# Kernel tuning notes

Hardware: AMD Instinct MI355X
Metric: run time of the kernel (lower is better)

Reference implementation:

```python
import jax, jax.numpy as jnp
import numpy as np

N_NODES = 50000
N_EDGES = 1600000
IN_DIM = 256
HID = 128
HEADS = 1
N_CLASSES = 40
NEG_SLOPE = 0.2


def gat_conv(x, W, a_src, a_dst, b, src, dst, concat):
    """PyG GATConv (eval mode). x: [N, F_in]; W: [H*C, F_in]; a_*: [H, C]; b: bias."""
    N = x.shape[0]
    H, C = a_src.shape
    h = (x @ W.T).reshape(N, H, C)                       # [N, H, C]
    alpha_src = jnp.sum(h * a_src, axis=-1)              # [N, H]
    alpha_dst = jnp.sum(h * a_dst, axis=-1)              # [N, H]
    e = jax.nn.leaky_relu(alpha_src[src] + alpha_dst[dst], NEG_SLOPE)  # [E, H]
    # scatter-softmax over incoming edges of each destination node
    m = jax.ops.segment_max(e, dst, num_segments=N)
    m = jnp.where(jnp.isfinite(m), m, 0.0)               # nodes with no in-edges
    ex = jnp.exp(e - m[dst])
    denom = jax.ops.segment_sum(ex, dst, num_segments=N)
    alpha = ex / jnp.maximum(denom[dst], 1e-16)          # [E, H]
    out = jax.ops.segment_sum(h[src] * alpha[..., None], dst, num_segments=N)  # [N, H, C]
    out = out.reshape(N, H * C) if concat else out.mean(axis=1)
    return out + b


def setup_inputs() -> dict:
    key = jax.random.key(0)
    ks = jax.random.split(key, 10)
    glorot = lambda k, shape: jax.random.normal(k, shape, jnp.float32) * np.sqrt(2.0 / (shape[0] + shape[-1]))
    x = jax.random.normal(ks[0], (N_NODES, IN_DIM), jnp.float32)
    edge_index = jax.random.randint(ks[1], (2, N_EDGES), 0, N_NODES, jnp.int64)
    # layer 0: in=IN_DIM -> hidden, heads=HEADS, concat=True
    W0 = glorot(ks[2], (HEADS * HID, IN_DIM))
    a_src0 = glorot(ks[3], (HEADS, HID))
    a_dst0 = glorot(ks[4], (HEADS, HID))
    b0 = jnp.zeros((HEADS * HID,), jnp.float32)
    # layer 1: in=hidden*heads -> n_classes, concat=False
    W1 = glorot(ks[5], (HEADS * N_CLASSES, HEADS * HID))
    a_src1 = glorot(ks[6], (HEADS, N_CLASSES))
    a_dst1 = glorot(ks[7], (HEADS, N_CLASSES))
    b1 = jnp.zeros((N_CLASSES,), jnp.float32)
    return {"x": x, "edge_index": edge_index,
            "W0": W0, "a_src0": a_src0, "a_dst0": a_dst0, "b0": b0,
            "W1": W1, "a_src1": a_src1, "a_dst1": a_dst1, "b1": b1}


def reference(x, edge_index, W0, a_src0, a_dst0, b0, W1, a_src1, a_dst1, b1):
    N = x.shape[0]
    # PyG GATConv default add_self_loops=True (each layer adds them transiently)
    loop = jnp.arange(N, dtype=edge_index.dtype)
    src = jnp.concatenate([edge_index[0], loop])
    dst = jnp.concatenate([edge_index[1], loop])
    h = gat_conv(x, W0, a_src0, a_dst0, b0, src, dst, concat=True)
    h = jax.nn.relu(h)  # dropout is identity in eval mode
    out = gat_conv(h, W1, a_src1, a_dst1, b1, src, dst, concat=False)
    return out
```

## Files before the change

kernel.cpp:

```cpp
#include <hip/hip_runtime.h>
#include <hip/hip_bf16.h>

#define N_NODES 50000
#define N_EDGES 1600000
#define ET (N_EDGES + N_NODES)
#define IN_DIM 256
#define HID 128
#define NCLS 40
#define NEG 0.2f
#define NBUCK 391
#define CHUNK 8192
#define CAP 5120

typedef short bf16x8 __attribute__((ext_vector_type(8)));
typedef float f32x4  __attribute__((ext_vector_type(4)));

__device__ __forceinline__ unsigned pk2(float a, float b) {
    __hip_bfloat16 ha = __float2bfloat16(a), hb = __float2bfloat16(b);
    unsigned short ua = *(unsigned short*)&ha, ub = *(unsigned short*)&hb;
    return (unsigned)ua | ((unsigned)ub << 16);
}
__device__ __forceinline__ float blo(unsigned u) { return __uint_as_float(u << 16); }
__device__ __forceinline__ float bhi(unsigned u) { return __uint_as_float(u & 0xffff0000u); }

__global__ void k_init(int* __restrict__ cursor) {
    int i = blockIdx.x * 256 + threadIdx.x;
    if (i < NBUCK) cursor[i] = i * CAP;
}

__global__ __launch_bounds__(256) void k_bin_scatter(const int* __restrict__ ei,
                                                     int* __restrict__ cursor,
                                                     unsigned int* __restrict__ buf) {
    __shared__ int sd[CHUNK];
    __shared__ int hist[NBUCK];
    __shared__ int wbase[NBUCK];
    int t = threadIdx.x;
    for (int i = t; i < NBUCK; i += 256) hist[i] = 0;
    __syncthreads();
    int base = blockIdx.x * CHUNK;
    #pragma unroll
    for (int j = 0; j < 32; ++j) {
        int i = base + j * 256 + t;
        int d = -1;
        if (i < ET) d = (i < N_EDGES) ? ei[N_EDGES + i] : (i - N_EDGES);
        sd[j * 256 + t] = d;
        if (d >= 0) atomicAdd(&hist[d >> 7], 1);
    }
    __syncthreads();
    for (int i = t; i < NBUCK; i += 256) {
        int h = hist[i];
        wbase[i] = h ? atomicAdd(&cursor[i], h) : 0;
        hist[i] = 0;
    }
    __syncthreads();
    #pragma unroll
    for (int j = 0; j < 32; ++j) {
        int i = base + j * 256 + t;
        int d = sd[j * 256 + t];
        if (d >= 0) {
            int s_ = (i < N_EDGES) ? ei[i] : d;
            int b = d >> 7;
            int off = atomicAdd(&hist[b], 1);
            buf[wbase[b] + off] = ((unsigned)(d & 127) << 16) | (unsigned)s_;
        }
    }
}

__global__ __launch_bounds__(512) void k_bin_scan(const int* __restrict__ cursor,
                                                  int* __restrict__ cstart,
                                                  int* __restrict__ rp) {
    __shared__ int s[512];
    int t = threadIdx.x;
    int v = (t < NBUCK) ? (cursor[t] - t * CAP) : 0;
    s[t] = v;
    __syncthreads();
    for (int off = 1; off < 512; off <<= 1) {
        int u = (t >= off) ? s[t - off] : 0;
        __syncthreads();
        s[t] += u;
        __syncthreads();
    }
    int ex = s[t] - v;
    if (t < NBUCK) cstart[t] = ex;
    if (t == 0) rp[N_NODES] = ET;
}

__global__ __launch_bounds__(256) void k_bucket_build(const unsigned int* __restrict__ buf,
                                                      const int* __restrict__ cursor,
                                                      const int* __restrict__ cstart,
                                                      int* __restrict__ rp,
                                                      int* __restrict__ csr) {
    __shared__ int cnt[128], rpl[128], cur[128];
    int b = blockIdx.x;
    int t = threadIdx.x;
    int lo = b * CAP, hi = cursor[b];
    int g = cstart[b];
    if (t < 128) cnt[t] = 0;
    __syncthreads();
    for (int i = lo + t; i < hi; i += 256) atomicAdd(&cnt[buf[i] >> 16], 1);
    __syncthreads();
    if (t == 0) {
        int run = 0;
        #pragma unroll
        for (int l = 0; l < 128; ++l) { rpl[l] = run; run += cnt[l]; }
    }
    __syncthreads();
    if (t < 128) {
        int node = b * 128 + t;
        if (node < N_NODES) rp[node] = g + rpl[t];
        cur[t] = 0;
    }
    __syncthreads();
    for (int i = lo + t; i < hi; i += 256) {
        unsigned v = buf[i];
        int dl = v >> 16;
        int off = atomicAdd(&cur[dl], 1);
        csr[g + rpl[dl] + off] = (int)(v & 0xffffu);
    }
}

__global__ __launch_bounds__(256) void k_gemm0(
    const float* __restrict__ x, const float* __restrict__ W0,
    const float* __restrict__ a_s, const float* __restrict__ a_d,
    unsigned short* __restrict__ h0b, float* __restrict__ as0, float* __restrict__ ad0) {
    __shared__ unsigned sA[64 * 36];
    __shared__ unsigned sB[128 * 36];
    int t = threadIdx.x;
    int n0 = blockIdx.x * 64;
    int w = t >> 6, lane = t & 63;
    int rw = lane & 15, q = lane >> 4;
    f32x4 acc[8];
    #pragma unroll
    for (int n = 0; n < 8; ++n) acc[n] = (f32x4){0.f, 0.f, 0.f, 0.f};

    for (int kc = 0; kc < IN_DIM; kc += 64) {
        #pragma unroll
        for (int i = 0; i < 4; ++i) {
            int f = i * 256 + t;
            int r = f >> 4, fq = f & 15;
            float4 v = make_float4(0.f, 0.f, 0.f, 0.f);
            if (n0 + r < N_NODES)
                v = *(const float4*)&x[(size_t)(n0 + r) * IN_DIM + kc + fq * 4];
            *(uint2*)&sA[r * 36 + fq * 2] = make_uint2(pk2(v.x, v.y), pk2(v.z, v.w));
        }
        #pragma unroll
        for (int i = 0; i < 8; ++i) {
            int f = i * 256 + t;
            int c = f >> 4, fq = f & 15;
            float4 v = *(const float4*)&W0[(size_t)c * IN_DIM + kc + fq * 4];
            *(uint2*)&sB[c * 36 + fq * 2] = make_uint2(pk2(v.x, v.y), pk2(v.z, v.w));
        }
        __syncthreads();
        #pragma unroll
        for (int ks = 0; ks < 2; ++ks) {
            bf16x8 af = *(const bf16x8*)((const unsigned short*)sA + (16 * w + rw) * 72 + ks * 32 + q * 8);
            #pragma unroll
            for (int n = 0; n < 8; ++n) {
                bf16x8 bfr = *(const bf16x8*)((const unsigned short*)sB + (n * 16 + rw) * 72 + ks * 32 + q * 8);
                acc[n] = __builtin_amdgcn_mfma_f32_16x16x32_bf16(af, bfr, acc[n], 0, 0, 0);
            }
        }
        __syncthreads();
    }

    float asv[8], adv[8];
    #pragma unroll
    for (int n = 0; n < 8; ++n) { asv[n] = a_s[n * 16 + rw]; adv[n] = a_d[n * 16 + rw]; }
    float ps[4] = {0.f, 0.f, 0.f, 0.f}, pd[4] = {0.f, 0.f, 0.f, 0.f};
    #pragma unroll
    for (int n = 0; n < 8; ++n)
        #pragma unroll
        for (int reg = 0; reg < 4; ++reg) {
            float vv = acc[n][reg];
            ps[reg] += vv * asv[n];
            pd[reg] += vv * adv[n];
        }
    #pragma unroll
    for (int reg = 0; reg < 4; ++reg) {
        int node = n0 + 16 * w + q * 4 + reg;
        if (node < N_NODES) {
            #pragma unroll
            for (int n = 0; n < 8; ++n) {
                __hip_bfloat16 hb = __float2bfloat16(acc[n][reg]);
                h0b[(size_t)node * HID + n * 16 + rw] = *(unsigned short*)&hb;
            }
        }
    }
    #pragma unroll
    for (int reg = 0; reg < 4; ++reg)
        #pragma unroll
        for (int off = 1; off < 16; off <<= 1) {
            ps[reg] += __shfl_xor(ps[reg], off);
            pd[reg] += __shfl_xor(pd[reg], off);
        }
    if (rw == 0) {
        #pragma unroll
        for (int reg = 0; reg < 4; ++reg) {
            int node = n0 + 16 * w + q * 4 + reg;
            if (node < N_NODES) { as0[node] = ps[reg]; ad0[node] = pd[reg]; }
        }
    }
}

__global__ __launch_bounds__(256) void k_agg0(
    const uint4* __restrict__ h0q, const float* __restrict__ as, const float* __restrict__ ad,
    const int* __restrict__ rp, const int* __restrict__ csr,
    const float* __restrict__ bias, unsigned short* __restrict__ actb) {
    __shared__ float sw_[4][64];
    __shared__ int   ss_[4][64];
    int wid = threadIdx.x >> 6, lane = threadIdx.x & 63;
    int q = lane >> 4, ql = lane & 15;
    int node = blockIdx.x * 4 + wid;
    int start = rp[node], end = rp[node + 1];
    float ad_n = ad[node];
    float a0 = 0.f, a1 = 0.f, a2 = 0.f, a3 = 0.f;
    float a4 = 0.f, a5 = 0.f, a6 = 0.f, a7 = 0.f, den = 0.f;
    for (int base = start; base < end; base += 64) {
        int mm = end - base; if (mm > 64) mm = 64;
        int s_l = 0; float w_l = 0.f;
        if (lane < mm) {
            s_l = csr[base + lane];
            float e = as[s_l] + ad_n;
            e = (e > 0.f) ? e : NEG * e;
            w_l = __expf(e);
            den += w_l;
        }
        ss_[wid][lane] = s_l;
        sw_[wid][lane] = w_l;
        for (int jj = 0; jj < mm; jj += 16) {
            int i0 = jj + q, i1 = i0 + 4, i2 = i0 + 8, i3 = i0 + 12;
            int   s0 = ss_[wid][i0], s1 = ss_[wid][i1], s2 = ss_[wid][i2], s3 = ss_[wid][i3];
            float w0 = sw_[wid][i0], w1 = sw_[wid][i1], w2 = sw_[wid][i2], w3 = sw_[wid][i3];
            uint4 u0 = h0q[(size_t)s0 * 16 + ql];
            uint4 u1 = h0q[(size_t)s1 * 16 + ql];
            uint4 u2 = h0q[(size_t)s2 * 16 + ql];
            uint4 u3 = h0q[(size_t)s3 * 16 + ql];
            a0 += w0 * blo(u0.x) + w1 * blo(u1.x) + w2 * blo(u2.x) + w3 * blo(u3.x);
            a1 += w0 * bhi(u0.x) + w1 * bhi(u1.x) + w2 * bhi(u2.x) + w3 * bhi(u3.x);
            a2 += w0 * blo(u0.y) + w1 * blo(u1.y) + w2 * blo(u2.y) + w3 * blo(u3.y);
            a3 += w0 * bhi(u0.y) + w1 * bhi(u1.y) + w2 * bhi(u2.y) + w3 * bhi(u3.y);
            a4 += w0 * blo(u0.z) + w1 * blo(u1.z) + w2 * blo(u2.z) + w3 * blo(u3.z);
            a5 += w0 * bhi(u0.z) + w1 * bhi(u1.z) + w2 * bhi(u2.z) + w3 * bhi(u3.z);
            a6 += w0 * blo(u0.w) + w1 * blo(u1.w) + w2 * blo(u2.w) + w3 * blo(u3.w);
            a7 += w0 * bhi(u0.w) + w1 * bhi(u1.w) + w2 * bhi(u2.w) + w3 * bhi(u3.w);
        }
    }
    #pragma unroll
    for (int off = 32; off; off >>= 1) den += __shfl_xor(den, off);
    a0 += __shfl_xor(a0, 16); a0 += __shfl_xor(a0, 32);
    a1 += __shfl_xor(a1, 16); a1 += __shfl_xor(a1, 32);
    a2 += __shfl_xor(a2, 16); a2 += __shfl_xor(a2, 32);
    a3 += __shfl_xor(a3, 16); a3 += __shfl_xor(a3, 32);
    a4 += __shfl_xor(a4, 16); a4 += __shfl_xor(a4, 32);
    a5 += __shfl_xor(a5, 16); a5 += __shfl_xor(a5, 32);
    a6 += __shfl_xor(a6, 16); a6 += __shfl_xor(a6, 32);
    a7 += __shfl_xor(a7, 16); a7 += __shfl_xor(a7, 32);
    if (lane < 16) {
        float inv = 1.f / fmaxf(den, 1e-16f);
        float4 b0v = *(const float4*)&bias[ql * 8];
        float4 b1v = *(const float4*)&bias[ql * 8 + 4];
        float r0 = fmaxf(a0 * inv + b0v.x, 0.f);
        float r1 = fmaxf(a1 * inv + b0v.y, 0.f);
        float r2 = fmaxf(a2 * inv + b0v.z, 0.f);
        float r3 = fmaxf(a3 * inv + b0v.w, 0.f);
        float r4 = fmaxf(a4 * inv + b1v.x, 0.f);
        float r5 = fmaxf(a5 * inv + b1v.y, 0.f);
        float r6 = fmaxf(a6 * inv + b1v.z, 0.f);
        float r7 = fmaxf(a7 * inv + b1v.w, 0.f);
        *(uint4*)&actb[(size_t)node * HID + ql * 8] =
            make_uint4(pk2(r0, r1), pk2(r2, r3), pk2(r4, r5), pk2(r6, r7));
    }
}

__global__ __launch_bounds__(128) void k_gemm1(
    const unsigned short* __restrict__ actb, const float* __restrict__ W1,
    const float* __restrict__ a_s, const float* __restrict__ a_d,
    unsigned short* __restrict__ h1b, float* __restrict__ as1, float* __restrict__ ad1) {
    __shared__ float w1l[NCLS * HID];
    __shared__ float av[NCLS], adv[NCLS];
    int t = threadIdx.x;
    #pragma unroll
    for (int i = 0; i < 10; ++i) {
        int j = t + 128 * i;
        ((float4*)w1l)[j] = ((const float4*)W1)[j];
    }
    if (t < NCLS) { av[t] = a_s[t]; adv[t] = a_d[t]; }
    __syncthreads();
    int n = blockIdx.x * 128 + t;
    if (n >= N_NODES) return;
    const uint4* ar = (const uint4*)(actb + (size_t)n * HID);
    float acc[NCLS];
    #pragma unroll
    for (int c = 0; c < NCLS; ++c) acc[c] = 0.f;
    for (int k0 = 0; k0 < HID; k0 += 8) {
        uint4 v = ar[k0 >> 3];
        float x0 = blo(v.x), x1 = bhi(v.x), x2 = blo(v.y), x3 = bhi(v.y);
        float x4 = blo(v.z), x5 = bhi(v.z), x6 = blo(v.w), x7 = bhi(v.w);
        #pragma unroll
        for (int c = 0; c < NCLS; ++c) {
            const float* wr = &w1l[c * HID + k0];
            acc[c] += x0 * wr[0] + x1 * wr[1] + x2 * wr[2] + x3 * wr[3]
                    + x4 * wr[4] + x5 * wr[5] + x6 * wr[6] + x7 * wr[7];
        }
    }
    float ps = 0.f, pd = 0.f;
    #pragma unroll
    for (int c = 0; c < NCLS; ++c) { ps += acc[c] * av[c]; pd += acc[c] * adv[c]; }
    unsigned pk_[20];
    #pragma unroll
    for (int c = 0; c < 20; ++c) pk_[c] = pk2(acc[2 * c], acc[2 * c + 1]);
    #pragma unroll
    for (int i = 0; i < 5; ++i)
        *(uint4*)&h1b[(size_t)n * NCLS + i * 8] = make_uint4(pk_[4*i], pk_[4*i+1], pk_[4*i+2], pk_[4*i+3]);
    as1[n] = ps; ad1[n] = pd;
}

__global__ __launch_bounds__(256) void k_agg1(
    const uint2* __restrict__ h1u, const float* __restrict__ as, const float* __restrict__ ad,
    const int* __restrict__ rp, const int* __restrict__ csr,
    const float* __restrict__ bias, float* __restrict__ out) {
    __shared__ float sw_[4][64];
    __shared__ int   ss_[4][64];
    int wid = threadIdx.x >> 6, lane = threadIdx.x & 63;
    int q = lane >> 4, ql = lane & 15;
    int off10 = (ql < 10) ? ql : 0;
    int node = blockIdx.x * 4 + wid;
    int start = rp[node], end = rp[node + 1];
    float ad_n = ad[node];
    float a0 = 0.f, a1 = 0.f, a2 = 0.f, a3 = 0.f, den = 0.f;
    for (int base = start; base < end; base += 64) {
        int mm = end - base; if (mm > 64) mm = 64;
        int s_l = 0; float w_l = 0.f;
        if (lane < mm) {
            s_l = csr[base + lane];
            float e = as[s_l] + ad_n;
            e = (e > 0.f) ? e : NEG * e;
            w_l = __expf(e);
            den += w_l;
        }
        ss_[wid][lane] = s_l;
        sw_[wid][lane] = w_l;
        for (int jj = 0; jj < mm; jj += 16) {
            int i0 = jj + q, i1 = i0 + 4, i2 = i0 + 8, i3 = i0 + 12;
            int   s0 = ss_[wid][i0], s1 = ss_[wid][i1], s2 = ss_[wid][i2], s3 = ss_[wid][i3];
            float w0 = sw_[wid][i0], w1 = sw_[wid][i1], w2 = sw_[wid][i2], w3 = sw_[wid][i3];
            uint2 u0 = h1u[(size_t)s0 * 10 + off10];
            uint2 u1 = h1u[(size_t)s1 * 10 + off10];
            uint2 u2 = h1u[(size_t)s2 * 10 + off10];
            uint2 u3 = h1u[(size_t)s3 * 10 + off10];
            a0 += w0 * blo(u0.x) + w1 * blo(u1.x) + w2 * blo(u2.x) + w3 * blo(u3.x);
            a1 += w0 * bhi(u0.x) + w1 * bhi(u1.x) + w2 * bhi(u2.x) + w3 * bhi(u3.x);
            a2 += w0 * blo(u0.y) + w1 * blo(u1.y) + w2 * blo(u2.y) + w3 * blo(u3.y);
            a3 += w0 * bhi(u0.y) + w1 * bhi(u1.y) + w2 * bhi(u2.y) + w3 * bhi(u3.y);
        }
    }
    #pragma unroll
    for (int off = 32; off; off >>= 1) den += __shfl_xor(den, off);
    a0 += __shfl_xor(a0, 16); a0 += __shfl_xor(a0, 32);
    a1 += __shfl_xor(a1, 16); a1 += __shfl_xor(a1, 32);
    a2 += __shfl_xor(a2, 16); a2 += __shfl_xor(a2, 32);
    a3 += __shfl_xor(a3, 16); a3 += __shfl_xor(a3, 32);
    if (lane < 10) {
        float inv = 1.f / fmaxf(den, 1e-16f);
        float4 b4 = *(const float4*)&bias[ql * 4];
        float4 r;
        r.x = a0 * inv + b4.x;
        r.y = a1 * inv + b4.y;
        r.z = a2 * inv + b4.z;
        r.w = a3 * inv + b4.w;
        *(float4*)&out[(size_t)node * NCLS + ql * 4] = r;
    }
}

extern "C" void kernel_launch(void* const* d_in, const int* in_sizes, int n_in,
                              void* d_out, int out_size, void* d_ws, size_t ws_size,
                              hipStream_t stream) {
    const float* x    = (const float*)d_in[0];
    const int*   ei   = (const int*)d_in[1];
    const float* W0   = (const float*)d_in[2];
    const float* a_s0 = (const float*)d_in[3];
    const float* a_d0 = (const float*)d_in[4];
    const float* b0   = (const float*)d_in[5];
    const float* W1   = (const float*)d_in[6];
    const float* a_s1 = (const float*)d_in[7];
    const float* a_d1 = (const float*)d_in[8];
    const float* b1   = (const float*)d_in[9];

    char* p = (char*)d_ws;
    auto alloc = [&](size_t bytes) { void* q = p; p += (bytes + 255) & ~size_t(255); return q; };
    unsigned short* h0b = (unsigned short*)alloc((size_t)N_NODES * HID * 2);
    unsigned int*   buf = (unsigned int*)h0b;
    unsigned short* h1b = (unsigned short*)alloc(((size_t)N_NODES * NCLS + 32) * 2);
    unsigned short* actb = (unsigned short*)alloc((size_t)N_NODES * HID * 2);
    float* as0    = (float*)alloc((size_t)N_NODES * 4);
    float* ad0    = (float*)alloc((size_t)N_NODES * 4);
    float* as1    = (float*)alloc((size_t)N_NODES * 4);
    float* ad1    = (float*)alloc((size_t)N_NODES * 4);
    int*   rp     = (int*)alloc((size_t)(N_NODES + 1) * 4);
    int*   csr    = (int*)alloc((size_t)ET * 4);
    int*   cstart = (int*)alloc((size_t)(NBUCK + 1) * 4);
    int*   cursor = (int*)alloc((size_t)NBUCK * 4);

    k_init<<<(NBUCK + 255) / 256, 256, 0, stream>>>(cursor);
    k_bin_scatter<<<(ET + CHUNK - 1) / CHUNK, 256, 0, stream>>>(ei, cursor, buf);
    k_bin_scan<<<1, 512, 0, stream>>>(cursor, cstart, rp);
    k_bucket_build<<<NBUCK, 256, 0, stream>>>(buf, cursor, cstart, rp, csr);
    k_gemm0<<<(N_NODES + 63) / 64, 256, 0, stream>>>(x, W0, a_s0, a_d0, h0b, as0, ad0);
    k_agg0<<<N_NODES / 4, 256, 0, stream>>>((const uint4*)h0b, as0, ad0, rp, csr, b0, actb);
    k_gemm1<<<(N_NODES + 127) / 128, 128, 0, stream>>>(actb, W1, a_s1, a_d1, h1b, as1, ad1);
    k_agg1<<<N_NODES / 4, 256, 0, stream>>>((const uint2*)h1b, as1, ad1, rp, csr, b1, (float*)d_out);
}
```

Before: 284.4 us.

## Fuse edge binning with layer-0 GEMM and drop global scan using padded CSR

Merges the edge-bin scatter and the layer-0 GEMM into one launch, with separate block ranges sharing a single LDS pool, so the memory-bound scatter and the compute-bound GEMM run concurrently. Removes the single-block scan kernel by laying out the CSR in fixed-capacity per-bucket slots and storing explicit per-node start and end arrays. Halves the scatter chunk size to get more blocks. In exchange, buf can no longer alias h0b and the CSR takes padded memory, which adds workspace and makes agg reads less contiguous.

```diff
diff --git a/kernel.cpp b/kernel.cpp
--- a/kernel.cpp
+++ b/kernel.cpp
@@ -9,8 +9,10 @@
 #define NCLS 40
 #define NEG 0.2f
 #define NBUCK 391
-#define CHUNK 8192
+#define CHUNK 4096
 #define CAP 5120
+#define SCATB ((ET + CHUNK - 1) / CHUNK)
+#define GEMMB ((N_NODES + 63) / 64)
 
 typedef short bf16x8 __attribute__((ext_vector_type(8)));
 typedef float f32x4  __attribute__((ext_vector_type(4)));
@@ -28,105 +30,53 @@
     if (i < NBUCK) cursor[i] = i * CAP;
 }
 
-__global__ __launch_bounds__(256) void k_bin_scatter(const int* __restrict__ ei,
-                                                     int* __restrict__ cursor,
-                                                     unsigned int* __restrict__ buf) {
-    __shared__ int sd[CHUNK];
-    __shared__ int hist[NBUCK];
-    __shared__ int wbase[NBUCK];
-    int t = threadIdx.x;
-    for (int i = t; i < NBUCK; i += 256) hist[i] = 0;
-    __syncthreads();
-    int base = blockIdx.x * CHUNK;
-    #pragma unroll
-    for (int j = 0; j < 32; ++j) {
-        int i = base + j * 256 + t;
-        int d = -1;
-        if (i < ET) d = (i < N_EDGES) ? ei[N_EDGES + i] : (i - N_EDGES);
-        sd[j * 256 + t] = d;
-        if (d >= 0) atomicAdd(&hist[d >> 7], 1);
-    }
-    __syncthreads();
-    for (int i = t; i < NBUCK; i += 256) {
-        int h = hist[i];
-        wbase[i] = h ? atomicAdd(&cursor[i], h) : 0;
-        hist[i] = 0;
-    }
-    __syncthreads();
-    #pragma unroll
-    for (int j = 0; j < 32; ++j) {
-        int i = base + j * 256 + t;
-        int d = sd[j * 256 + t];
-        if (d >= 0) {
-            int s_ = (i < N_EDGES) ? ei[i] : d;
-            int b = d >> 7;
-            int off = atomicAdd(&hist[b], 1);
-            buf[wbase[b] + off] = ((unsigned)(d & 127) << 16) | (unsigned)s_;
-        }
-    }
-}
-
-__global__ __launch_bounds__(512) void k_bin_scan(const int* __restrict__ cursor,
-                                                  int* __restrict__ cstart,
-                                                  int* __restrict__ rp) {
-    __shared__ int s[512];
-    int t = threadIdx.x;
-    int v = (t < NBUCK) ? (cursor[t] - t * CAP) : 0;
-    s[t] = v;
-    __syncthreads();
-    for (int off = 1; off < 512; off <<= 1) {
-        int u = (t >= off) ? s[t - off] : 0;
-        __syncthreads();
-        s[t] += u;
-        __syncthreads();
-    }
-    int ex = s[t] - v;
-    if (t < NBUCK) cstart[t] = ex;
-    if (t == 0) rp[N_NODES] = ET;
-}
-
-__global__ __launch_bounds__(256) void k_bucket_build(const unsigned int* __restrict__ buf,
-                                                      const int* __restrict__ cursor,
-                                                      const int* __restrict__ cstart,
-                                                      int* __restrict__ rp,
-                                                      int* __restrict__ csr) {
-    __shared__ int cnt[128], rpl[128], cur[128];
-    int b = blockIdx.x;
-    int t = threadIdx.x;
-    int lo = b * CAP, hi = cursor[b];
-    int g = cstart[b];
-    if (t < 128) cnt[t] = 0;
-    __syncthreads();
-    for (int i = lo + t; i < hi; i += 256) atomicAdd(&cnt[buf[i] >> 16], 1);
-    __syncthreads();
-    if (t == 0) {
-        int run = 0;
-        #pragma unroll
-        for (int l = 0; l < 128; ++l) { rpl[l] = run; run += cnt[l]; }
-    }
-    __syncthreads();
-    if (t < 128) {
-        int node = b * 128 + t;
-        if (node < N_NODES) rp[node] = g + rpl[t];
-        cur[t] = 0;
-    }
-    __syncthreads();
-    for (int i = lo + t; i < hi; i += 256) {
-        unsigned v = buf[i];
-        int dl = v >> 16;
-        int off = atomicAdd(&cur[dl], 1);
-        csr[g + rpl[dl] + off] = (int)(v & 0xffffu);
-    }
-}
-
-__global__ __launch_bounds__(256) void k_gemm0(
+__global__ __launch_bounds__(256) void k_fused(
+    const int* __restrict__ ei, int* __restrict__ cursor, unsigned int* __restrict__ buf,
     const float* __restrict__ x, const float* __restrict__ W0,
     const float* __restrict__ a_s, const float* __restrict__ a_d,
     unsigned short* __restrict__ h0b, float* __restrict__ as0, float* __restrict__ ad0) {
-    __shared__ unsigned sA[64 * 36];
-    __shared__ unsigned sB[128 * 36];
+    __shared__ unsigned pool[6912];
     int t = threadIdx.x;
-    int n0 = blockIdx.x * 64;
+
+    if (blockIdx.x < SCATB) {
+        int* sd    = (int*)pool;
+        int* hist  = (int*)pool + 4096;
+        int* wbase = (int*)pool + 4487;
+        for (int i = t; i < NBUCK; i += 256) hist[i] = 0;
+        __syncthreads();
+        int base = blockIdx.x * CHUNK;
+        #pragma unroll
+        for (int j = 0; j < 16; ++j) {
+            int i = base + j * 256 + t;
+            int d = -1;
+            if (i < ET) d = (i < N_EDGES) ? ei[N_EDGES + i] : (i - N_EDGES);
+            sd[j * 256 + t] = d;
+            if (d >= 0) atomicAdd(&hist[d >> 7], 1);
+        }
+        __syncthreads();
+        for (int i = t; i < NBUCK; i += 256) {
+            int h = hist[i];
+            wbase[i] = h ? atomicAdd(&cursor[i], h) : 0;
+            hist[i] = 0;
+        }
+        __syncthreads();
+        #pragma unroll
+        for (int j = 0; j < 16; ++j) {
+            int i = base + j * 256 + t;
+            int d = sd[j * 256 + t];
+            if (d >= 0) {
+                int s_ = (i < N_EDGES) ? ei[i] : d;
+                int b = d >> 7;
+                int off = atomicAdd(&hist[b], 1);
+                buf[wbase[b] + off] = ((unsigned)(d & 127) << 16) | (unsigned)s_;
+            }
+        }
+        return;
+    }
+
+    unsigned* sA = pool;
+    unsigned* sB = pool + 2304;
+    int n0 = (blockIdx.x - SCATB) * 64;
     int w = t >> 6, lane = t & 63;
     int rw = lane & 15, q = lane >> 4;
     f32x4 acc[8];
@@ -202,16 +152,48 @@
     }
 }
 
+__global__ __launch_bounds__(256) void k_bucket_build(const unsigned int* __restrict__ buf,
+                                                      const int* __restrict__ cursor,
+                                                      int* __restrict__ rp, int* __restrict__ re,
+                                                      int* __restrict__ csr) {
+    __shared__ int cnt[128], rpl[128], cur[128];
+    int b = blockIdx.x;
+    int t = threadIdx.x;
+    int lo = b * CAP, hi = cursor[b];
+    if (t < 128) cnt[t] = 0;
+    __syncthreads();
+    for (int i = lo + t; i < hi; i += 256) atomicAdd(&cnt[buf[i] >> 16], 1);
+    __syncthreads();
+    if (t == 0) {
+        int run = 0;
+        #pragma unroll
+        for (int l = 0; l < 128; ++l) { rpl[l] = run; run += cnt[l]; }
+    }
+    __syncthreads();
+    if (t < 128) {
+        int node = b * 128 + t;
+        if (node < N_NODES) { rp[node] = lo + rpl[t]; re[node] = lo + rpl[t] + cnt[t]; }
+        cur[t] = 0;
+    }
+    __syncthreads();
+    for (int i = lo + t; i < hi; i += 256) {
+        unsigned v = buf[i];
+        int dl = v >> 16;
+        int off = atomicAdd(&cur[dl], 1);
+        csr[lo + rpl[dl] + off] = (int)(v & 0xffffu);
+    }
+}
+
 __global__ __launch_bounds__(256) void k_agg0(
     const uint4* __restrict__ h0q, const float* __restrict__ as, const float* __restrict__ ad,
-    const int* __restrict__ rp, const int* __restrict__ csr,
+    const int* __restrict__ rp, const int* __restrict__ re, const int* __restrict__ csr,
     const float* __restrict__ bias, unsigned short* __restrict__ actb) {
     __shared__ float sw_[4][64];
     __shared__ int   ss_[4][64];
     int wid = threadIdx.x >> 6, lane = threadIdx.x & 63;
     int q = lane >> 4, ql = lane & 15;
     int node = blockIdx.x * 4 + wid;
-    int start = rp[node], end = rp[node + 1];
+    int start = rp[node], end = re[node];
     float ad_n = ad[node];
     float a0 = 0.f, a1 = 0.f, a2 = 0.f, a3 = 0.f;
     float a4 = 0.f, a5 = 0.f, a6 = 0.f, a7 = 0.f, den = 0.f;
@@ -317,7 +299,7 @@
 
 __global__ __launch_bounds__(256) void k_agg1(
     const uint2* __restrict__ h1u, const float* __restrict__ as, const float* __restrict__ ad,
-    const int* __restrict__ rp, const int* __restrict__ csr,
+    const int* __restrict__ rp, const int* __restrict__ re, const int* __restrict__ csr,
     const float* __restrict__ bias, float* __restrict__ out) {
     __shared__ float sw_[4][64];
     __shared__ int   ss_[4][64];
@@ -325,7 +307,7 @@
     int q = lane >> 4, ql = lane & 15;
     int off10 = (ql < 10) ? ql : 0;
     int node = blockIdx.x * 4 + wid;
-    int start = rp[node], end = rp[node + 1];
+    int start = rp[node], end = re[node];
     float ad_n = ad[node];
     float a0 = 0.f, a1 = 0.f, a2 = 0.f, a3 = 0.f, den = 0.f;
     for (int base = start; base < end; base += 64) {
@@ -388,25 +370,23 @@
 
     char* p = (char*)d_ws;
     auto alloc = [&](size_t bytes) { void* q = p; p += (bytes + 255) & ~size_t(255); return q; };
-    unsigned short* h0b = (unsigned short*)alloc((size_t)N_NODES * HID * 2);
-    unsigned int*   buf = (unsigned int*)h0b;
-    unsigned short* h1b = (unsigned short*)alloc(((size_t)N_NODES * NCLS + 32) * 2);
+    unsigned short* h0b  = (unsigned short*)alloc((size_t)N_NODES * HID * 2);
+    unsigned int*   buf  = (unsigned int*)alloc((size_t)NBUCK * CAP * 4);
+    int*   csr    = (int*)alloc((size_t)NBUCK * CAP * 4);
+    unsigned short* h1b  = (unsigned short*)alloc(((size_t)N_NODES * NCLS + 32) * 2);
     unsigned short* actb = (unsigned short*)alloc((size_t)N_NODES * HID * 2);
     float* as0    = (float*)alloc((size_t)N_NODES * 4);
     float* ad0    = (float*)alloc((size_t)N_NODES * 4);
     float* as1    = (float*)alloc((size_t)N_NODES * 4);
     float* ad1    = (float*)alloc((size_t)N_NODES * 4);
-    int*   rp     = (int*)alloc((size_t)(N_NODES + 1) * 4);
-    int*   csr    = (int*)alloc((size_t)ET * 4);
-    int*   cstart = (int*)alloc((size_t)(NBUCK + 1) * 4);
+    int*   rp     = (int*)alloc((size_t)N_NODES * 4);
+    int*   re     = (int*)alloc((size_t)N_NODES * 4);
     int*   cursor = (int*)alloc((size_t)NBUCK * 4);
 
     k_init<<<(NBUCK + 255) / 256, 256, 0, stream>>>(cursor);
-    k_bin_scatter<<<(ET + CHUNK - 1) / CHUNK, 256, 0, stream>>>(ei, cursor, buf);
-    k_bin_scan<<<1, 512, 0, stream>>>(cursor, cstart, rp);
-    k_bucket_build<<<NBUCK, 256, 0, stream>>>(buf, cursor, cstart, rp, csr);
-    k_gemm0<<<(N_NODES + 63) / 64, 256, 0, stream>>>(x, W0, a_s0, a_d0, h0b, as0, ad0);
-    k_agg0<<<N_NODES / 4, 256, 0, stream>>>((const uint4*)h0b, as0, ad0, rp, csr, b0, actb);
+    k_fused<<<SCATB + GEMMB, 256, 0, stream>>>(ei, cursor, buf, x, W0, a_s0, a_d0, h0b, as0, ad0);
+    k_bucket_build<<<NBUCK, 256, 0, stream>>>(buf, cursor, rp, re, csr);
+    k_agg0<<<N_NODES / 4, 256, 0, stream>>>((const uint4*)h0b, as0, ad0, rp, re, csr, b0, actb);
     k_gemm1<<<(N_NODES + 127) / 128, 128, 0, stream>>>(actb, W1, a_s1, a_d1, h1b, as1, ad1);
-    k_agg1<<<N_NODES / 4, 256, 0, stream>>>((const uint2*)h1b, as1, ad1, rp, csr, b1, (float*)d_out);
-}
+    k_agg1<<<N_NODES / 4, 256, 0, stream>>>((const uint2*)h1b, as1, ad1, rp, re, csr, b1, (float*)d_out);
+}
```

Result: faster. 271.3 us (-4.6%).
